# Performance work log

Hardware: AMD Instinct MI355X
Metric: run time of the kernel (lower is better)

Reference implementation:

```python
import jax, jax.numpy as jnp
import numpy as np
import math
from jax import lax

HIDDEN = 512
BETA = 1.0
MAX_ITERATIONS = 5
CONV_THRESH = 1e-4
SCALE = BETA / math.sqrt(HIDDEN)


def setup_inputs() -> dict:
    key = jax.random.key(0)
    ks = jax.random.split(key, 9)
    B, S, H = 4, 2048, HIDDEN
    w = 1.0 / math.sqrt(H)  # roughly nn.Linear init scale
    return {
        "x": jax.random.normal(ks[0], (B, S, H), jnp.float32),
        "Wq": jax.random.normal(ks[1], (H, H), jnp.float32) * w,
        "bq": jax.random.normal(ks[2], (H,), jnp.float32) * w,
        "Wk": jax.random.normal(ks[3], (H, H), jnp.float32) * w,
        "bk": jax.random.normal(ks[4], (H,), jnp.float32) * w,
        "Wv": jax.random.normal(ks[5], (H, H), jnp.float32) * w,
        "bv": jax.random.normal(ks[6], (H,), jnp.float32) * w,
        "Wo": jax.random.normal(ks[7], (H, H), jnp.float32) * w,
        "bo": jax.random.normal(ks[8], (H,), jnp.float32) * w,
    }


def _hopfield_update(state, keys):
    # scores: [B, S, S]
    scores = jnp.einsum('bsh,bth->bst', state, keys) * SCALE
    attn = jax.nn.softmax(scores, axis=-1)
    return jnp.einsum('bst,bth->bsh', attn, keys)


def reference(x, Wq, bq, Wk, bk, Wv, bv, Wo, bo):
    query = x @ Wq.T + bq
    keys = x @ Wk.T + bk
    values = x @ Wv.T + bv

    # Iterative Hopfield loop: torch breaks after the update that converges.
    # We run a fixed-length scan, freezing state once converged (same math).
    def step(carry, _):
        state, converged, iters = carry
        new_state = _hopfield_update(state, keys)
        # global Frobenius norms, matching torch.norm over the whole tensor
        delta = jnp.linalg.norm(new_state - state) / (jnp.linalg.norm(state) + 1e-8)
        active = jnp.logical_not(converged)
        state = jnp.where(active, new_state, state)
        iters = iters + active.astype(jnp.int32)
        converged = converged | (active & (delta < CONV_THRESH))
        return (state, converged, iters), None

    init = (query, jnp.array(False), jnp.array(0, jnp.int32))
    (state, converged, iterations), _ = lax.scan(step, init, None, length=MAX_ITERATIONS)

    # Final readout attention against values
    scores = jnp.einsum('bsh,bth->bst', state, keys) * SCALE
    attn = jax.nn.softmax(scores, axis=-1)
    out = jnp.einsum('bst,bth->bsh', attn, values)
    out = out @ Wo.T + bo  # dropout p=0.0 / eval: identity
    return out, iterations, converged
```

## Files before the change

### kernel.cpp

```cpp
#include <hip/hip_runtime.h>
#include <hip/hip_bf16.h>
#include <math.h>

#define HH 512
#define BB 4
#define SS 2048
#define NN (BB*SS)
#define SCALE_F 0.04419417382415922f
#define THRESH 1e-4f
#define CTL_FLOATS 1024

typedef __attribute__((ext_vector_type(8))) short bf16x8;
typedef __attribute__((ext_vector_type(4))) float f32x4;

struct Ctl { float sum_d; float sum_o; int iters; int conv; int cur; int bf[10]; };

__device__ __forceinline__ float b2f(unsigned short u) {
    union { unsigned int i; float f; } c; c.i = ((unsigned int)u) << 16; return c.f;
}
__device__ __forceinline__ unsigned short f2b(float f) {
    unsigned int x = __float_as_uint(f);
    unsigned int r = (x + 0x7FFFu + ((x >> 16) & 1u)) >> 16;
    return (unsigned short)r;
}
__device__ __forceinline__ void splitf(float x, unsigned short& h, unsigned short& l) {
    h = f2b(x);
    l = f2b(x - b2f(h));
}
__device__ __forceinline__ f32x4 MF(bf16x8 a, bf16x8 b, f32x4 c) {
    return __builtin_amdgcn_mfma_f32_16x16x32_bf16(a, b, c, 0, 0, 0);
}

#define FBAR() do { \
    asm volatile("s_waitcnt lgkmcnt(0)" ::: "memory"); \
    __builtin_amdgcn_s_barrier(); \
    asm volatile("" ::: "memory"); \
} while (0)

#define LD8(R, ph, pl) do { \
    const unsigned short* _ph = (ph); const unsigned short* _pl = (pl); \
    R##0 = *(const uint4*)(_ph);      R##1 = *(const uint4*)(_ph + 8); \
    R##2 = *(const uint4*)(_ph + 16); R##3 = *(const uint4*)(_ph + 24); \
    R##4 = *(const uint4*)(_pl);      R##5 = *(const uint4*)(_pl + 8); \
    R##6 = *(const uint4*)(_pl + 16); R##7 = *(const uint4*)(_pl + 24); \
} while (0)
#define ST8(dh, dl, R) do { \
    unsigned short* _dh = (dh); unsigned short* _dl = (dl); \
    *(uint4*)(_dh)      = R##0; *(uint4*)(_dh + 8)  = R##1; \
    *(uint4*)(_dh + 16) = R##2; *(uint4*)(_dh + 24) = R##3; \
    *(uint4*)(_dl)      = R##4; *(uint4*)(_dl + 8)  = R##5; \
    *(uint4*)(_dl + 16) = R##6; *(uint4*)(_dl + 24) = R##7; \
} while (0)

__global__ __launch_bounds__(256) void detect_dtypes(
        const void* p0, const void* p1, const void* p2, const void* p3, const void* p4,
        const void* p5, const void* p6, const void* p7, const void* p8, Ctl* sc)
{
    const void* ps[9] = {p0,p1,p2,p3,p4,p5,p6,p7,p8};
    const int   ns[9] = {NN*HH, HH*HH, HH, HH*HH, HH, HH*HH, HH, HH*HH, HH};
    const int i = blockIdx.x;
    const unsigned short* u = (const unsigned short*)ps[i];
    const int n = ns[i] < 4096 ? ns[i] : 4096;
    __shared__ int cnt;
    if (threadIdx.x == 0) cnt = 0;
    __syncthreads();
    int c = 0;
    for (int j = threadIdx.x; j < n; j += 256) {
        const int e = (u[j] >> 7) & 0xFF;
        if (e < 32 || e >= 224) ++c;
    }
    if (c) atomicAdd(&cnt, c);
    __syncthreads();
    if (threadIdx.x == 0) sc->bf[i] = (cnt * 16 < n) ? 1 : 0;
}

__global__ __launch_bounds__(64) void init_flags(Ctl* sc) {
    if (threadIdx.x == 0) {
        sc->iters = 0; sc->conv = 0; sc->cur = 0; sc->sum_d = 0.f; sc->sum_o = 0.f;
        int any = 0;
        for (int i = 0; i < 9; ++i) any |= sc->bf[i];
        sc->bf[9] = any;
    }
}

__global__ __launch_bounds__(256) void mfma_gemm(
    const void* __restrict__ Xv, int xIdx,
    const void* __restrict__ Wv, int wIdx,
    const void* __restrict__ Bv, int bIdx,
    float* __restrict__ outF, void* __restrict__ outExt,
    unsigned short* __restrict__ pKH, unsigned short* __restrict__ pKL,
    unsigned short* __restrict__ pKTH, unsigned short* __restrict__ pKTL,
    float* __restrict__ S0w, float* __restrict__ S1w,
    int mode, const Ctl* __restrict__ sc)
{
    __shared__ unsigned short Xh[64][72], Xl[64][72], Wh[64][72], Wl[64][72];
    const int tid = threadIdx.x;
    const int cur = sc->cur;
    const void* Xp = (xIdx == -2) ? (const void*)(cur ? S1w : S0w) : Xv;
    const bool xbf = (xIdx >= 0) && (sc->bf[xIdx] != 0);
    const bool wbf = (sc->bf[wIdx] != 0);
    const bool bbf = (sc->bf[bIdx] != 0);
    const bool obf = (mode == 1) && (sc->bf[9] != 0);
    const bool xs = !xbf, ws = !wbf;

    const int m0 = blockIdx.x * 64, n0 = blockIdx.y * 64;
    const int lane = tid & 63, w = tid >> 6;
    const int mi = w & 1, ni = w >> 1;
    const int quad = lane >> 4, l16 = lane & 15;
    const int srow = tid >> 2, skb = (tid & 3) * 16;

    f32x4 acc[2][2];
    #pragma unroll
    for (int a = 0; a < 2; ++a)
        #pragma unroll
        for (int bq = 0; bq < 2; ++bq) acc[a][bq] = (f32x4){0.f, 0.f, 0.f, 0.f};

    for (int kc = 0; kc < HH; kc += 64) {
        __syncthreads();
        {
            float v[16];
            if (xbf) {
                const unsigned short* p = (const unsigned short*)Xp + (size_t)(m0 + srow)*HH + kc + skb;
                #pragma unroll
                for (int i = 0; i < 4; ++i) {
                    ushort4 t = *(const ushort4*)(p + 4*i);
                    v[4*i]=b2f(t.x); v[4*i+1]=b2f(t.y); v[4*i+2]=b2f(t.z); v[4*i+3]=b2f(t.w);
                }
            } else {
                const float* p = (const float*)Xp + (size_t)(m0 + srow)*HH + kc + skb;
                #pragma unroll
                for (int i = 0; i < 4; ++i) {
                    float4 t = *(const float4*)(p + 4*i);
                    v[4*i]=t.x; v[4*i+1]=t.y; v[4*i+2]=t.z; v[4*i+3]=t.w;
                }
            }
            #pragma unroll
            for (int i = 0; i < 4; ++i) {
                unsigned short h[4], l[4];
                #pragma unroll
                for (int j = 0; j < 4; ++j) splitf(v[4*i+j], h[j], l[j]);
                *(ushort4*)&Xh[srow][skb + 4*i] = make_ushort4(h[0], h[1], h[2], h[3]);
                if (xs) *(ushort4*)&Xl[srow][skb + 4*i] = make_ushort4(l[0], l[1], l[2], l[3]);
            }
        }
        {
            float v[16];
            if (wbf) {
                const unsigned short* p = (const unsigned short*)Wv + (size_t)(n0 + srow)*HH + kc + skb;
                #pragma unroll
                for (int i = 0; i < 4; ++i) {
                    ushort4 t = *(const ushort4*)(p + 4*i);
                    v[4*i]=b2f(t.x); v[4*i+1]=b2f(t.y); v[4*i+2]=b2f(t.z); v[4*i+3]=b2f(t.w);
                }
            } else {
                const float* p = (const float*)Wv + (size_t)(n0 + srow)*HH + kc + skb;
                #pragma unroll
                for (int i = 0; i < 4; ++i) {
                    float4 t = *(const float4*)(p + 4*i);
                    v[4*i]=t.x; v[4*i+1]=t.y; v[4*i+2]=t.z; v[4*i+3]=t.w;
                }
            }
            #pragma unroll
            for (int i = 0; i < 4; ++i) {
                unsigned short h[4], l[4];
                #pragma unroll
                for (int j = 0; j < 4; ++j) splitf(v[4*i+j], h[j], l[j]);
                *(ushort4*)&Wh[srow][skb + 4*i] = make_ushort4(h[0], h[1], h[2], h[3]);
                if (ws) *(ushort4*)&Wl[srow][skb + 4*i] = make_ushort4(l[0], l[1], l[2], l[3]);
            }
        }
        __syncthreads();
        #pragma unroll
        for (int d = 0; d < 2; ++d) {
            const int kl = 32*d + quad*8;
            #pragma unroll
            for (int mt = 0; mt < 2; ++mt) {
                const int xr = 32*mi + 16*mt + l16;
                bf16x8 ahx = *(const bf16x8*)&Xh[xr][kl];
                bf16x8 alx;
                if (xs) alx = *(const bf16x8*)&Xl[xr][kl];
                #pragma unroll
                for (int nt = 0; nt < 2; ++nt) {
                    const int wr = 32*ni + 16*nt + l16;
                    bf16x8 bh = *(const bf16x8*)&Wh[wr][kl];
                    acc[mt][nt] = MF(ahx, bh, acc[mt][nt]);
                    if (xs) acc[mt][nt] = MF(alx, bh, acc[mt][nt]);
                    if (ws) {
                        bf16x8 bl = *(const bf16x8*)&Wl[wr][kl];
                        acc[mt][nt] = MF(ahx, bl, acc[mt][nt]);
                    }
                }
            }
        }
    }
    unsigned short* vtH = nullptr;
    if (mode == 4) { vtH = (unsigned short*)(cur ? S0w : S1w); }
    #pragma unroll
    for (int nt = 0; nt < 2; ++nt) {
        const int col = n0 + 32*ni + 16*nt + l16;
        const float bv = bbf ? b2f(((const unsigned short*)Bv)[col]) : ((const float*)Bv)[col];
        #pragma unroll
        for (int mt = 0; mt < 2; ++mt)
            #pragma unroll
            for (int e = 0; e < 4; ++e) {
                const int row = m0 + 32*mi + 16*mt + quad*4 + e;
                const float vv = acc[mt][nt][e] + bv;
                const size_t idx = (size_t)row*HH + col;
                if (mode == 0) outF[idx] = vv;
                else if (mode == 1) {
                    if (obf) ((unsigned short*)outExt)[idx] = f2b(vv);
                    else     ((float*)outExt)[idx] = vv;
                } else {
                    unsigned short h, l; splitf(vv, h, l);
                    const size_t t = ((size_t)(row >> 11) * HH + col) * SS + (row & 2047);
                    if (mode == 3) {
                        pKH[idx] = h; pKL[idx] = l;
                        pKTH[t] = h;  pKTL[t] = l;
                    } else {
                        vtH[t] = h; vtH[(size_t)NN*HH + t] = l;
                    }
                }
            }
    }
}

template<bool FINAL>
__global__ __launch_bounds__(256, 1) void mfma_attn(
    float* __restrict__ S0w, float* __restrict__ S1w,
    const unsigned short* __restrict__ KH, const unsigned short* __restrict__ KL,
    const unsigned short* __restrict__ KTH, const unsigned short* __restrict__ KTL,
    Ctl* sc)
{
    if constexpr (!FINAL) { if (sc->conv) return; }
    const int cur = sc->cur;
    float* Scur = cur ? S1w : S0w;
    float* Out  = FINAL ? Scur : (cur ? S0w : S1w);
    const unsigned short* VTH = FINAL ? (const unsigned short*)(cur ? S0w : S1w) : KTH;
    const unsigned short* VTL = FINAL ? (VTH + (size_t)NN*HH) : KTL;

    __shared__ __align__(16) unsigned short UB0[18432];
    __shared__ __align__(16) unsigned short UB1[18432];
    __shared__ __align__(16) unsigned short SHl[32*520];
    __shared__ __align__(16) unsigned short Pth[32*72], Ptl[32*72];
    __shared__ __align__(16) float Sld[32*68];
    __shared__ __align__(16) float mld[32], lld[32], ald[32];
    __shared__ float redd[4], redo[4];

    const int tid = threadIdx.x;
    const int lane = tid & 63, w = tid >> 6;
    const int quad = lane >> 4, l16 = lane & 15;
    const int r = w & 1, s = w >> 1;

    const int bid = blockIdx.x;
    const int e8 = bid & 7;
    const int b = e8 >> 1;
    const int q0 = 32 * ((bid >> 3) + 32 * (e8 & 1));

    const size_t bSSHH = (size_t)b * SS * HH;
    const size_t bHHSS = (size_t)b * HH * SS;

    const int key = tid >> 2, hs = (tid & 3) * 32;
    const int rw = tid >> 1, k1 = (tid & 1) * 32;

    const unsigned short* pSH = KH + bSSHH + (size_t)key*HH + hs;
    const unsigned short* pSL = KL + bSSHH + (size_t)key*HH + hs;
    const size_t vbase = bHHSS + (size_t)((rw & 63) + 256*(rw >> 6))*SS + k1;
    const unsigned short* pVH = VTH + vbase;
    const unsigned short* pVL = VTL + vbase;

    uint4 Ra0, Ra1, Ra2, Ra3, Ra4, Ra5, Ra6, Ra7;
    uint4 Rb0, Rb1, Rb2, Rb3, Rb4, Rb5, Rb6, Rb7;
    LD8(Ra, pSH, pSL);
    LD8(Rb, pSH + 128, pSL + 128);

    bf16x8 ah[16];
    {
        const float* Qr = Scur + ((size_t)b*SS + q0 + 16*r + l16) * HH + quad*8;
        #pragma unroll
        for (int f = 0; f < 16; ++f) {
            float4 v0 = *(const float4*)(Qr + 32*f);
            float4 v1 = *(const float4*)(Qr + 32*f + 4);
            unsigned short h[8], l[8];
            splitf(v0.x,h[0],l[0]); splitf(v0.y,h[1],l[1]); splitf(v0.z,h[2],l[2]); splitf(v0.w,h[3],l[3]);
            splitf(v1.x,h[4],l[4]); splitf(v1.y,h[5],l[5]); splitf(v1.z,h[6],l[6]); splitf(v1.w,h[7],l[7]);
            bf16x8 af;
            #pragma unroll
            for (int j = 0; j < 8; ++j) af[j] = (short)h[j];
            ah[f] = af;
            if (s == 0) {
                unsigned short* d = &SHl[(16*r + l16)*520 + 32*f + quad*8];
                *(ushort4*)(d)     = make_ushort4(l[0], l[1], l[2], l[3]);
                *(ushort4*)(d + 4) = make_ushort4(l[4], l[5], l[6], l[7]);
            }
        }
        if (tid < 32) { mld[tid] = -INFINITY; lld[tid] = 0.f; }
    }

    f32x4 O[16];
    #pragma unroll
    for (int i = 0; i < 16; ++i) O[i] = (f32x4){0.f, 0.f, 0.f, 0.f};

    for (int kt = 0; kt < SS/64; ++kt) {
        const size_t so = (size_t)kt*64*HH;
        const size_t po = (size_t)kt*64;
        f32x4 sA0 = (f32x4){0.f,0.f,0.f,0.f}, sB0 = (f32x4){0.f,0.f,0.f,0.f};
        f32x4 sA1 = (f32x4){0.f,0.f,0.f,0.f}, sB1 = (f32x4){0.f,0.f,0.f,0.f};
        #pragma unroll
        for (int c = 0; c < 4; ++c) {
            unsigned short* ub = (c & 1) ? UB1 : UB0;
            if ((c & 1) == 0) {
                ST8(ub + key*136 + hs, ub + 8704 + key*136 + hs, Ra);
                if (c == 0) LD8(Ra, pSH + so + 2*128, pSL + so + 2*128);
                else        LD8(Ra, pVH + po, pVL + po);
            } else {
                ST8(ub + key*136 + hs, ub + 8704 + key*136 + hs, Rb);
                if (c == 1) LD8(Rb, pSH + so + 3*128, pSL + so + 3*128);
                else        LD8(Rb, pVH + (size_t)64*SS + po, pVL + (size_t)64*SS + po);
            }
            FBAR();
            #pragma unroll
            for (int kf = 0; kf < 4; ++kf) {
                bf16x8 alf = *(const bf16x8*)&SHl[(16*r + l16)*520 + c*128 + kf*32 + quad*8];
                const int c0 = kf*32 + quad*8;
                const unsigned short* BH = ub;
                const unsigned short* BL = ub + 8704;
                bf16x8 bh0 = *(const bf16x8*)&BH[(32*s + l16)*136 + c0];
                bf16x8 bl0 = *(const bf16x8*)&BL[(32*s + l16)*136 + c0];
                bf16x8 bh1 = *(const bf16x8*)&BH[(32*s + 16 + l16)*136 + c0];
                bf16x8 bl1 = *(const bf16x8*)&BL[(32*s + 16 + l16)*136 + c0];
                const bf16x8 a = ah[c*4 + kf];
                if (kf & 1) {
                    sB0 = MF(a, bh0, sB0); sB0 = MF(alf, bh0, sB0); sB0 = MF(a, bl0, sB0);
                    sB1 = MF(a, bh1, sB1); sB1 = MF(alf, bh1, sB1); sB1 = MF(a, bl1, sB1);
                } else {
                    sA0 = MF(a, bh0, sA0); sA0 = MF(alf, bh0, sA0); sA0 = MF(a, bl0, sA0);
                    sA1 = MF(a, bh1, sA1); sA1 = MF(alf, bh1, sA1); sA1 = MF(a, bl1, sA1);
                }
            }
        }
        f32x4 sacc0 = sA0 + sB0;
        f32x4 sacc1 = sA1 + sB1;
        #pragma unroll
        for (int e = 0; e < 4; ++e) {
            Sld[(16*r + quad*4 + e)*68 + 32*s + l16]      = sacc0[e] * SCALE_F;
            Sld[(16*r + quad*4 + e)*68 + 32*s + 16 + l16] = sacc1[e] * SCALE_F;
        }
        FBAR();
        {
            const int row = tid >> 3, sg = tid & 7;
            const float* sr = Sld + row*68 + sg*8;
            float4 x0 = *(const float4*)(sr);
            float4 x1 = *(const float4*)(sr + 4);
            float mt = fmaxf(fmaxf(fmaxf(x0.x,x0.y), fmaxf(x0.z,x0.w)),
                             fmaxf(fmaxf(x1.x,x1.y), fmaxf(x1.z,x1.w)));
            #pragma unroll
            for (int mk = 1; mk < 8; mk <<= 1) mt = fmaxf(mt, __shfl_xor(mt, mk, 8));
            const float mprev = mld[row];
            const float mnew = fmaxf(mprev, mt);
            float p[8];
            p[0]=__expf(x0.x-mnew); p[1]=__expf(x0.y-mnew); p[2]=__expf(x0.z-mnew); p[3]=__expf(x0.w-mnew);
            p[4]=__expf(x1.x-mnew); p[5]=__expf(x1.y-mnew); p[6]=__expf(x1.z-mnew); p[7]=__expf(x1.w-mnew);
            float ps = p[0]+p[1]+p[2]+p[3]+p[4]+p[5]+p[6]+p[7];
            #pragma unroll
            for (int mk = 1; mk < 8; mk <<= 1) ps += __shfl_xor(ps, mk, 8);
            const float alpha = __expf(mprev - mnew);
            if (sg == 0) { mld[row] = mnew; lld[row] = lld[row]*alpha + ps; ald[row] = alpha; }
            unsigned short h[8], l[8];
            #pragma unroll
            for (int i = 0; i < 8; ++i) splitf(p[i], h[i], l[i]);
            unsigned short* dh = &Pth[row*72 + sg*8];
            unsigned short* dl = &Ptl[row*72 + sg*8];
            *(ushort4*)(dh)     = make_ushort4(h[0],h[1],h[2],h[3]);
            *(ushort4*)(dh + 4) = make_ushort4(h[4],h[5],h[6],h[7]);
            *(ushort4*)(dl)     = make_ushort4(l[0],l[1],l[2],l[3]);
            *(ushort4*)(dl + 4) = make_ushort4(l[4],l[5],l[6],l[7]);
        }
        FBAR();
        {
            const float4 av = *(const float4*)&ald[16*r + 4*quad];
            const float a4[4] = {av.x, av.y, av.z, av.w};
            #pragma unroll
            for (int i = 0; i < 16; ++i)
                #pragma unroll
                for (int e = 0; e < 4; ++e) O[i][e] *= a4[e];
        }
        bf16x8 pah[2], pal[2];
        #pragma unroll
        for (int kf = 0; kf < 2; ++kf) {
            pah[kf] = *(const bf16x8*)&Pth[(16*r + l16)*72 + kf*32 + quad*8];
            pal[kf] = *(const bf16x8*)&Ptl[(16*r + l16)*72 + kf*32 + quad*8];
        }
        #pragma unroll
        for (int c = 0; c < 4; ++c) {
            unsigned short* ub = (c & 1) ? UB1 : UB0;
            if ((c & 1) == 0) {
                ST8(ub + rw*72 + k1, ub + 9216 + rw*72 + k1, Ra);
                if (c == 0)             LD8(Ra, pVH + (size_t)2*64*SS + po, pVL + (size_t)2*64*SS + po);
                else if (kt+1 < SS/64)  LD8(Ra, pSH + so + (size_t)64*HH,
                                             pSL + so + (size_t)64*HH);
            } else {
                ST8(ub + rw*72 + k1, ub + 9216 + rw*72 + k1, Rb);
                if (c == 1)             LD8(Rb, pVH + (size_t)3*64*SS + po, pVL + (size_t)3*64*SS + po);
                else if (kt+1 < SS/64)  LD8(Rb, pSH + so + (size_t)64*HH + 128,
                                             pSL + so + (size_t)64*HH + 128);
            }
            FBAR();
            #pragma unroll
            for (int nt = 0; nt < 4; ++nt) {
                const int rb = (64*s + 16*nt + l16)*72;
                #pragma unroll
                for (int kf = 0; kf < 2; ++kf) {
                    bf16x8 bh = *(const bf16x8*)&ub[rb + kf*32 + quad*8];
                    bf16x8 bl = *(const bf16x8*)&ub[9216 + rb + kf*32 + quad*8];
                    O[c*4+nt] = MF(pah[kf], bh, O[c*4+nt]);
                    O[c*4+nt] = MF(pal[kf], bh, O[c*4+nt]);
                    O[c*4+nt] = MF(pah[kf], bl, O[c*4+nt]);
                }
            }
        }
    }
    const float4 lv = *(const float4*)&lld[16*r + 4*quad];
    const float inv[4] = {1.f/lv.x, 1.f/lv.y, 1.f/lv.z, 1.f/lv.w};
    float pd = 0.f, po2 = 0.f;
    #pragma unroll
    for (int c = 0; c < 4; ++c)
        #pragma unroll
        for (int nt = 0; nt < 4; ++nt)
            #pragma unroll
            for (int e = 0; e < 4; ++e) {
                const int row = q0 + 16*r + quad*4 + e;
                const int col = 256*s + 64*c + 16*nt + l16;
                const float nv = O[c*4+nt][e] * inv[e];
                const size_t idx = (size_t)b*SS*HH + (size_t)row*HH + col;
                if constexpr (!FINAL) {
                    const float old = Scur[idx];
                    const float d = nv - old;
                    pd += d*d; po2 += old*old;
                }
                Out[idx] = nv;
            }
    if constexpr (!FINAL) {
        #pragma unroll
        for (int mk = 1; mk < 64; mk <<= 1) {
            pd  += __shfl_xor(pd, mk, 64);
            po2 += __shfl_xor(po2, mk, 64);
        }
        if (lane == 0) { redd[w] = pd; redo[w] = po2; }
        __syncthreads();
        if (tid == 0) {
            atomicAdd(&sc->sum_d, redd[0] + redd[1] + redd[2] + redd[3]);
            atomicAdd(&sc->sum_o, redo[0] + redo[1] + redo[2] + redo[3]);
        }
    }
}

__global__ __launch_bounds__(64) void flag_update(Ctl* sc) {
    if (threadIdx.x != 0) return;
    if (sc->conv) return;
    sc->cur ^= 1;
    sc->iters += 1;
    const float delta = sqrtf(sc->sum_d) / (sqrtf(sc->sum_o) + 1e-8f);
    if (delta < THRESH) sc->conv = 1;
    sc->sum_d = 0.f; sc->sum_o = 0.f;
}

__global__ __launch_bounds__(64) void write_scalars(const Ctl* sc, void* outv) {
    if (threadIdx.x != 0) return;
    if (sc->bf[9]) {
        unsigned short* o = (unsigned short*)outv;
        o[(size_t)NN*HH]     = f2b((float)sc->iters);
        o[(size_t)NN*HH + 1] = f2b(sc->conv ? 1.0f : 0.0f);
    } else {
        float* o = (float*)outv;
        o[(size_t)NN*HH]     = (float)sc->iters;
        o[(size_t)NN*HH + 1] = sc->conv ? 1.0f : 0.0f;
    }
}

extern "C" void kernel_launch(void* const* d_in, const int* in_sizes, int n_in,
                              void* d_out, int out_size, void* d_ws, size_t ws_size,
                              hipStream_t stream)
{
    const void* x  = d_in[0];
    const void* Wq = d_in[1];
    const void* bq = d_in[2];
    const void* Wk = d_in[3];
    const void* bk = d_in[4];
    const void* Wv = d_in[5];
    const void* bv = d_in[6];
    const void* Wo = d_in[7];
    const void* bo = d_in[8];

    Ctl* sc = (Ctl*)d_ws;
    float* S0 = (float*)d_ws + CTL_FLOATS;
    float* S1 = S0 + (size_t)NN*HH;
    unsigned short* KH  = (unsigned short*)(S1 + (size_t)NN*HH);
    unsigned short* KL  = KH  + (size_t)NN*HH;
    unsigned short* KTH = KL  + (size_t)NN*HH;
    unsigned short* KTL = KTH + (size_t)NN*HH;

    const dim3 ggrid(NN/64, HH/64);
    const int  agrid = 256;

    detect_dtypes<<<9, 256, 0, stream>>>(x, Wq, bq, Wk, bk, Wv, bv, Wo, bo, sc);
    init_flags<<<1, 64, 0, stream>>>(sc);

    mfma_gemm<<<ggrid, 256, 0, stream>>>(x, 0, Wq, 1, bq, 2, S0, nullptr,
                                         nullptr, nullptr, nullptr, nullptr, S0, S1, 0, sc);
    mfma_gemm<<<ggrid, 256, 0, stream>>>(x, 0, Wk, 3, bk, 4, nullptr, nullptr,
                                         KH, KL, KTH, KTL, S0, S1, 3, sc);

    for (int it = 0; it < 5; ++it) {
        mfma_attn<false><<<agrid, 256, 0, stream>>>(S0, S1, KH, KL, KTH, KTL, sc);
        flag_update<<<1, 64, 0, stream>>>(sc);
    }

    mfma_gemm<<<ggrid, 256, 0, stream>>>(x, 0, Wv, 5, bv, 6, nullptr, nullptr,
                                         nullptr, nullptr, nullptr, nullptr, S0, S1, 4, sc);
    mfma_attn<true><<<agrid, 256, 0, stream>>>(S0, S1, KH, KL, KTH, KTL, sc);
    mfma_gemm<<<ggrid, 256, 0, stream>>>(nullptr, -2, Wo, 7, bo, 8, nullptr, d_out,
                                         nullptr, nullptr, nullptr, nullptr, S0, S1, 1, sc);
    if (out_size >= (int)((size_t)NN*HH + 2))
        write_scalars<<<1, 64, 0, stream>>>(sc, d_out);
}
```

Before: 1.532 ms.

## Double attention block to 512 threads, halving per-wave score and output tiles

The flash-style attention kernel now launches 512 threads (8 waves) per block instead of 256. The work is repartitioned: each wave computes a 16-key score slice and 8 output accumulator tiles instead of 16, and global-to-LDS staging loads shrink to 4 vectors per thread. Softmax is spread over 16 lanes per row, and the norm reduction sums 8 wave partials. The aim is more waves in flight per CU to hide memory and MFMA latency and to lower register pressure, at the cost of more barrier participants and smaller per-wave MFMA batches.

```diff
diff --git a/kernel.cpp b/kernel.cpp
--- a/kernel.cpp
+++ b/kernel.cpp
@@ -37,19 +37,15 @@
     asm volatile("" ::: "memory"); \
 } while (0)
 
-#define LD8(R, ph, pl) do { \
+#define LD4(R, ph, pl) do { \
     const unsigned short* _ph = (ph); const unsigned short* _pl = (pl); \
-    R##0 = *(const uint4*)(_ph);      R##1 = *(const uint4*)(_ph + 8); \
-    R##2 = *(const uint4*)(_ph + 16); R##3 = *(const uint4*)(_ph + 24); \
-    R##4 = *(const uint4*)(_pl);      R##5 = *(const uint4*)(_pl + 8); \
-    R##6 = *(const uint4*)(_pl + 16); R##7 = *(const uint4*)(_pl + 24); \
+    R##0 = *(const uint4*)(_ph); R##1 = *(const uint4*)(_ph + 8); \
+    R##2 = *(const uint4*)(_pl); R##3 = *(const uint4*)(_pl + 8); \
 } while (0)
-#define ST8(dh, dl, R) do { \
+#define ST4(dh, dl, R) do { \
     unsigned short* _dh = (dh); unsigned short* _dl = (dl); \
-    *(uint4*)(_dh)      = R##0; *(uint4*)(_dh + 8)  = R##1; \
-    *(uint4*)(_dh + 16) = R##2; *(uint4*)(_dh + 24) = R##3; \
-    *(uint4*)(_dl)      = R##4; *(uint4*)(_dl + 8)  = R##5; \
-    *(uint4*)(_dl + 16) = R##6; *(uint4*)(_dl + 24) = R##7; \
+    *(uint4*)(_dh) = R##0; *(uint4*)(_dh + 8) = R##1; \
+    *(uint4*)(_dl) = R##2; *(uint4*)(_dl + 8) = R##3; \
 } while (0)
 
 __global__ __launch_bounds__(256) void detect_dtypes(
@@ -225,7 +221,7 @@
 }
 
 template<bool FINAL>
-__global__ __launch_bounds__(256, 1) void mfma_attn(
+__global__ __launch_bounds__(512, 2) void mfma_attn(
     float* __restrict__ S0w, float* __restrict__ S1w,
     const unsigned short* __restrict__ KH, const unsigned short* __restrict__ KL,
     const unsigned short* __restrict__ KTH, const unsigned short* __restrict__ KTL,
@@ -244,7 +240,7 @@
     __shared__ __align__(16) unsigned short Pth[32*72], Ptl[32*72];
     __shared__ __align__(16) float Sld[32*68];
     __shared__ __align__(16) float mld[32], lld[32], ald[32];
-    __shared__ float redd[4], redo[4];
+    __shared__ float redd[8], redo[8];
 
     const int tid = threadIdx.x;
     const int lane = tid & 63, w = tid >> 6;
@@ -259,19 +255,19 @@
     const size_t bSSHH = (size_t)b * SS * HH;
     const size_t bHHSS = (size_t)b * HH * SS;
 
-    const int key = tid >> 2, hs = (tid & 3) * 32;
-    const int rw = tid >> 1, k1 = (tid & 1) * 32;
+    const int key = tid >> 3, hs = (tid & 7) * 16;
+    const int rw = tid >> 2, k1 = (tid & 3) * 16;
 
     const unsigned short* pSH = KH + bSSHH + (size_t)key*HH + hs;
     const unsigned short* pSL = KL + bSSHH + (size_t)key*HH + hs;
-    const size_t vbase = bHHSS + (size_t)((rw & 63) + 256*(rw >> 6))*SS + k1;
+    const size_t vbase = bHHSS + (size_t)(128*(rw >> 5) + (rw & 31))*SS + k1;
     const unsigned short* pVH = VTH + vbase;
     const unsigned short* pVL = VTL + vbase;
 
-    uint4 Ra0, Ra1, Ra2, Ra3, Ra4, Ra5, Ra6, Ra7;
-    uint4 Rb0, Rb1, Rb2, Rb3, Rb4, Rb5, Rb6, Rb7;
-    LD8(Ra, pSH, pSL);
-    LD8(Rb, pSH + 128, pSL + 128);
+    uint4 Ra0, Ra1, Ra2, Ra3;
+    uint4 Rb0, Rb1, Rb2, Rb3;
+    LD4(Ra, pSH, pSL);
+    LD4(Rb, pSH + 128, pSL + 128);
 
     bf16x8 ah[16];
     {
@@ -296,91 +292,76 @@
         if (tid < 32) { mld[tid] = -INFINITY; lld[tid] = 0.f; }
     }
 
-    f32x4 O[16];
+    f32x4 O[8];
     #pragma unroll
-    for (int i = 0; i < 16; ++i) O[i] = (f32x4){0.f, 0.f, 0.f, 0.f};
+    for (int i = 0; i < 8; ++i) O[i] = (f32x4){0.f, 0.f, 0.f, 0.f};
+
+    const int shlbase = (16*r + l16)*520 + quad*8;
 
     for (int kt = 0; kt < SS/64; ++kt) {
         const size_t so = (size_t)kt*64*HH;
         const size_t po = (size_t)kt*64;
-        f32x4 sA0 = (f32x4){0.f,0.f,0.f,0.f}, sB0 = (f32x4){0.f,0.f,0.f,0.f};
-        f32x4 sA1 = (f32x4){0.f,0.f,0.f,0.f}, sB1 = (f32x4){0.f,0.f,0.f,0.f};
+        f32x4 sA = (f32x4){0.f,0.f,0.f,0.f}, sB = (f32x4){0.f,0.f,0.f,0.f};
         #pragma unroll
         for (int c = 0; c < 4; ++c) {
             unsigned short* ub = (c & 1) ? UB1 : UB0;
             if ((c & 1) == 0) {
-                ST8(ub + key*136 + hs, ub + 8704 + key*136 + hs, Ra);
-                if (c == 0) LD8(Ra, pSH + so + 2*128, pSL + so + 2*128);
-                else        LD8(Ra, pVH + po, pVL + po);
+                ST4(ub + key*136 + hs, ub + 8704 + key*136 + hs, Ra);
+                if (c == 0) LD4(Ra, pSH + so + 2*128, pSL + so + 2*128);
+                else        LD4(Ra, pVH + po, pVL + po);
             } else {
-                ST8(ub + key*136 + hs, ub + 8704 + key*136 + hs, Rb);
-                if (c == 1) LD8(Rb, pSH + so + 3*128, pSL + so + 3*128);
-                else        LD8(Rb, pVH + (size_t)64*SS + po, pVL + (size_t)64*SS + po);
+                ST4(ub + key*136 + hs, ub + 8704 + key*136 + hs, Rb);
+                if (c == 1) LD4(Rb, pSH + so + 3*128, pSL + so + 3*128);
+                else        LD4(Rb, pVH + (size_t)32*SS + po, pVL + (size_t)32*SS + po);
             }
             FBAR();
             #pragma unroll
             for (int kf = 0; kf < 4; ++kf) {
-                bf16x8 alf = *(const bf16x8*)&SHl[(16*r + l16)*520 + c*128 + kf*32 + quad*8];
+                bf16x8 alf = *(const bf16x8*)&SHl[shlbase + c*128 + kf*32];
                 const int c0 = kf*32 + quad*8;
-                const unsigned short* BH = ub;
-                const unsigned short* BL = ub + 8704;
-                bf16x8 bh0 = *(const bf16x8*)&BH[(32*s + l16)*136 + c0];
-                bf16x8 bl0 = *(const bf16x8*)&BL[(32*s + l16)*136 + c0];
-                bf16x8 bh1 = *(const bf16x8*)&BH[(32*s + 16 + l16)*136 + c0];
-                bf16x8 bl1 = *(const bf16x8*)&BL[(32*s + 16 + l16)*136 + c0];
+                bf16x8 bh = *(const bf16x8*)&ub[(16*s + l16)*136 + c0];
+                bf16x8 bl = *(const bf16x8*)&ub[8704 + (16*s + l16)*136 + c0];
                 const bf16x8 a = ah[c*4 + kf];
                 if (kf & 1) {
-                    sB0 = MF(a, bh0, sB0); sB0 = MF(alf, bh0, sB0); sB0 = MF(a, bl0, sB0);
-                    sB1 = MF(a, bh1, sB1); sB1 = MF(alf, bh1, sB1); sB1 = MF(a, bl1, sB1);
+                    sB = MF(a, bh, sB); sB = MF(alf, bh, sB); sB = MF(a, bl, sB);
                 } else {
-                    sA0 = MF(a, bh0, sA0); sA0 = MF(alf, bh0, sA0); sA0 = MF(a, bl0, sA0);
-                    sA1 = MF(a, bh1, sA1); sA1 = MF(alf, bh1, sA1); sA1 = MF(a, bl1, sA1);
-                }
-            }
-        }
-        f32x4 sacc0 = sA0 + sB0;
-        f32x4 sacc1 = sA1 + sB1;
-        #pragma unroll
-        for (int e = 0; e < 4; ++e) {
-            Sld[(16*r + quad*4 + e)*68 + 32*s + l16]      = sacc0[e] * SCALE_F;
-            Sld[(16*r + quad*4 + e)*68 + 32*s + 16 + l16] = sacc1[e] * SCALE_F;
-        }
+                    sA = MF(a, bh, sA); sA = MF(alf, bh, sA); sA = MF(a, bl, sA);
+                }
+            }
+        }
+        f32x4 sacc = sA + sB;
+        #pragma unroll
+        for (int e = 0; e < 4; ++e)
+            Sld[(16*r + quad*4 + e)*68 + 16*s + l16] = sacc[e] * SCALE_F;
         FBAR();
         {
-            const int row = tid >> 3, sg = tid & 7;
-            const float* sr = Sld + row*68 + sg*8;
+            const int row = tid >> 4, sg = tid & 15;
+            const float* sr = Sld + row*68 + sg*4;
             float4 x0 = *(const float4*)(sr);
-            float4 x1 = *(const float4*)(sr + 4);
-            float mt = fmaxf(fmaxf(fmaxf(x0.x,x0.y), fmaxf(x0.z,x0.w)),
-                             fmaxf(fmaxf(x1.x,x1.y), fmaxf(x1.z,x1.w)));
-            #pragma unroll
-            for (int mk = 1; mk < 8; mk <<= 1) mt = fmaxf(mt, __shfl_xor(mt, mk, 8));
+            float mt = fmaxf(fmaxf(x0.x, x0.y), fmaxf(x0.z, x0.w));
+            #pragma unroll
+            for (int mk = 1; mk < 16; mk <<= 1) mt = fmaxf(mt, __shfl_xor(mt, mk, 16));
             const float mprev = mld[row];
             const float mnew = fmaxf(mprev, mt);
-            float p[8];
+            float p[4];
             p[0]=__expf(x0.x-mnew); p[1]=__expf(x0.y-mnew); p[2]=__expf(x0.z-mnew); p[3]=__expf(x0.w-mnew);
-            p[4]=__expf(x1.x-mnew); p[5]=__expf(x1.y-mnew); p[6]=__expf(x1.z-mnew); p[7]=__expf(x1.w-mnew);
-            float ps = p[0]+p[1]+p[2]+p[3]+p[4]+p[5]+p[6]+p[7];
-            #pragma unroll
-            for (int mk = 1; mk < 8; mk <<= 1) ps += __shfl_xor(ps, mk, 8);
+            float ps = p[0]+p[1]+p[2]+p[3];
+            #pragma unroll
+            for (int mk = 1; mk < 16; mk <<= 1) ps += __shfl_xor(ps, mk, 16);
             const float alpha = __expf(mprev - mnew);
             if (sg == 0) { mld[row] = mnew; lld[row] = lld[row]*alpha + ps; ald[row] = alpha; }
-            unsigned short h[8], l[8];
-            #pragma unroll
-            for (int i = 0; i < 8; ++i) splitf(p[i], h[i], l[i]);
-            unsigned short* dh = &Pth[row*72 + sg*8];
-            unsigned short* dl = &Ptl[row*72 + sg*8];
-            *(ushort4*)(dh)     = make_ushort4(h[0],h[1],h[2],h[3]);
-            *(ushort4*)(dh + 4) = make_ushort4(h[4],h[5],h[6],h[7]);
-            *(ushort4*)(dl)     = make_ushort4(l[0],l[1],l[2],l[3]);
-            *(ushort4*)(dl + 4) = make_ushort4(l[4],l[5],l[6],l[7]);
+            unsigned short h[4], l[4];
+            #pragma unroll
+            for (int i = 0; i < 4; ++i) splitf(p[i], h[i], l[i]);
+            *(ushort4*)&Pth[row*72 + sg*4] = make_ushort4(h[0],h[1],h[2],h[3]);
+            *(ushort4*)&Ptl[row*72 + sg*4] = make_ushort4(l[0],l[1],l[2],l[3]);
         }
         FBAR();
         {
             const float4 av = *(const float4*)&ald[16*r + 4*quad];
             const float a4[4] = {av.x, av.y, av.z, av.w};
             #pragma unroll
-            for (int i = 0; i < 16; ++i)
+            for (int i = 0; i < 8; ++i)
                 #pragma unroll
                 for (int e = 0; e < 4; ++e) O[i][e] *= a4[e];
         }
@@ -394,27 +375,27 @@
         for (int c = 0; c < 4; ++c) {
             unsigned short* ub = (c & 1) ? UB1 : UB0;
             if ((c & 1) == 0) {
-                ST8(ub + rw*72 + k1, ub + 9216 + rw*72 + k1, Ra);
-                if (c == 0)             LD8(Ra, pVH + (size_t)2*64*SS + po, pVL + (size_t)2*64*SS + po);
-                else if (kt+1 < SS/64)  LD8(Ra, pSH + so + (size_t)64*HH,
+                ST4(ub + rw*72 + k1, ub + 9216 + rw*72 + k1, Ra);
+                if (c == 0)             LD4(Ra, pVH + (size_t)64*SS + po, pVL + (size_t)64*SS + po);
+                else if (kt+1 < SS/64)  LD4(Ra, pSH + so + (size_t)64*HH,
                                              pSL + so + (size_t)64*HH);
             } else {
-                ST8(ub + rw*72 + k1, ub + 9216 + rw*72 + k1, Rb);
-                if (c == 1)             LD8(Rb, pVH + (size_t)3*64*SS + po, pVL + (size_t)3*64*SS + po);
-                else if (kt+1 < SS/64)  LD8(Rb, pSH + so + (size_t)64*HH + 128,
+                ST4(ub + rw*72 + k1, ub + 9216 + rw*72 + k1, Rb);
+                if (c == 1)             LD4(Rb, pVH + (size_t)96*SS + po, pVL + (size_t)96*SS + po);
+                else if (kt+1 < SS/64)  LD4(Rb, pSH + so + (size_t)64*HH + 128,
                                              pSL + so + (size_t)64*HH + 128);
             }
             FBAR();
             #pragma unroll
-            for (int nt = 0; nt < 4; ++nt) {
-                const int rb = (64*s + 16*nt + l16)*72;
+            for (int nt = 0; nt < 2; ++nt) {
+                const int rb = (32*s + 16*nt + l16)*72;
                 #pragma unroll
                 for (int kf = 0; kf < 2; ++kf) {
                     bf16x8 bh = *(const bf16x8*)&ub[rb + kf*32 + quad*8];
                     bf16x8 bl = *(const bf16x8*)&ub[9216 + rb + kf*32 + quad*8];
-                    O[c*4+nt] = MF(pah[kf], bh, O[c*4+nt]);
-                    O[c*4+nt] = MF(pal[kf], bh, O[c*4+nt]);
-                    O[c*4+nt] = MF(pah[kf], bl, O[c*4+nt]);
+                    O[c*2+nt] = MF(pah[kf], bh, O[c*2+nt]);
+                    O[c*2+nt] = MF(pal[kf], bh, O[c*2+nt]);
+                    O[c*2+nt] = MF(pah[kf], bl, O[c*2+nt]);
                 }
             }
         }
@@ -425,12 +406,12 @@
     #pragma unroll
     for (int c = 0; c < 4; ++c)
         #pragma unroll
-        for (int nt = 0; nt < 4; ++nt)
+        for (int nt = 0; nt < 2; ++nt)
             #pragma unroll
             for (int e = 0; e < 4; ++e) {
                 const int row = q0 + 16*r + quad*4 + e;
-                const int col = 256*s + 64*c + 16*nt + l16;
-                const float nv = O[c*4+nt][e] * inv[e];
+                const int col = 128*s + 32*c + 16*nt + l16;
+                const float nv = O[c*2+nt][e] * inv[e];
                 const size_t idx = (size_t)b*SS*HH + (size_t)row*HH + col;
                 if constexpr (!FINAL) {
                     const float old = Scur[idx];
@@ -448,8 +429,11 @@
         if (lane == 0) { redd[w] = pd; redo[w] = po2; }
         __syncthreads();
         if (tid == 0) {
-            atomicAdd(&sc->sum_d, redd[0] + redd[1] + redd[2] + redd[3]);
-            atomicAdd(&sc->sum_o, redo[0] + redo[1] + redo[2] + redo[3]);
+            float td = 0.f, to = 0.f;
+            #pragma unroll
+            for (int i = 0; i < 8; ++i) { td += redd[i]; to += redo[i]; }
+            atomicAdd(&sc->sum_d, td);
+            atomicAdd(&sc->sum_o, to);
         }
     }
 }
@@ -511,13 +495,13 @@
                                          KH, KL, KTH, KTL, S0, S1, 3, sc);
 
     for (int it = 0; it < 5; ++it) {
-        mfma_attn<false><<<agrid, 256, 0, stream>>>(S0, S1, KH, KL, KTH, KTL, sc);
+        mfma_attn<false><<<agrid, 512, 0, stream>>>(S0, S1, KH, KL, KTH, KTL, sc);
         flag_update<<<1, 64, 0, stream>>>(sc);
     }
 
     mfma_gemm<<<ggrid, 256, 0, stream>>>(x, 0, Wv, 5, bv, 6, nullptr, nullptr,
                                          nullptr, nullptr, nullptr, nullptr, S0, S1, 4, sc);
-    mfma_attn<true><<<agrid, 256, 0, stream>>>(S0, S1, KH, KL, KTH, KTL, sc);
+    mfma_attn<true><<<agrid, 512, 0, stream>>>(S0, S1, KH, KL, KTH, KTL, sc);
     mfma_gemm<<<ggrid, 256, 0, stream>>>(nullptr, -2, Wo, 7, bo, 8, nullptr, d_out,
                                          nullptr, nullptr, nullptr, nullptr, S0, S1, 1, sc);
     if (out_size >= (int)((size_t)NN*HH + 2))
```

Measured after the change: 1.277 ms. 1.2x faster.
